# Kernel tuning notes

Measured on AMD Instinct MI355X. Metric: run time of the kernel, lower is better.

Reference implementation:

```python
import jax, jax.numpy as jnp
import numpy as np

B, NF, E, T, M = 4096, 50, 64, 2, 3
LN_EPS = 1e-5
NEG_INF = -1e9


def _xavier_uniform(k, shape, fan_in, fan_out):
    a = float(np.sqrt(6.0 / (fan_in + fan_out)))
    return jax.random.uniform(k, shape, jnp.float32, -a, a)


def setup_inputs() -> dict:
    key = jax.random.key(0)
    ks = jax.random.split(key, 6)
    feat = jax.random.normal(ks[0], (B, NF, E), jnp.float32)
    masker = _xavier_uniform(ks[1], (T, M, NF, NF), NF, NF)
    transform_w = _xavier_uniform(ks[2], (1, T, 1, 2 * E, E), 2 * E, E)
    transform_b = _xavier_uniform(ks[3], (T, 1, NF, E), NF, E)
    ln_w = jnp.ones((NF,), jnp.float32)
    ln_b = jnp.zeros((NF,), jnp.float32)
    gating_w = jax.random.normal(ks[4], (NF * E, 1), jnp.float32) / np.sqrt(NF * E)
    gating_b = jnp.zeros((1,), jnp.float32)
    return {
        "feat": feat,
        "masker": masker,
        "transform_w": transform_w,
        "transform_b": transform_b,
        "ln_w": ln_w,
        "ln_b": ln_b,
        "gating_w": gating_w,
        "gating_b": gating_b,
    }


def reference(feat, masker, transform_w, transform_b, ln_w, ln_b, gating_w, gating_b):
    b, nf, e = feat.shape
    t = masker.shape[0]
    # hop adjacency: product of masks, relu'd  (T, F, F)
    adj = jax.nn.relu(jnp.prod(masker, axis=1))
    mask = (adj != 0).astype(feat.dtype)
    # LayerNorm(num_fields) applied on transposed adj == normalize over axis -2,
    # with gamma/beta broadcasting along the normalized (row) axis.
    mean = adj.mean(axis=-2, keepdims=True)
    var = adj.var(axis=-2, keepdims=True)
    adj_ln = (adj - mean) / jnp.sqrt(var + LN_EPS) * ln_w[:, None] + ln_b[:, None]
    logits = adj_ln + (1.0 - mask) * NEG_INF + jnp.eye(nf, dtype=feat.dtype)
    # softmax over dim=1 of (T, F, F) == axis -2 (rows), then re-mask
    attn = jax.nn.softmax(logits, axis=-2) * mask
    # nei[b,t,g,e] = sum_f feat[b,f,e] * attn[t,f,g]
    nei = jnp.einsum('bfe,tfg->btge', feat, attn)  # (B, T, F, E)
    x = jnp.broadcast_to(feat[:, None], (b, t, nf, e))
    cat = jnp.concatenate([x, nei], axis=-1)  # (B, T, F, 2E)
    w0 = transform_w[0, :, 0]                 # (T, 2E, E)  (idx=0 slice)
    h = jnp.einsum('btfk,tke->btfe', cat, w0) + transform_b[:, 0]  # (B,T,F,E)
    flat = h.reshape(b, t, nf * e)
    gate = jax.nn.softmax(flat @ gating_w + gating_b, axis=1)  # (B, T, 1)
    out = jnp.sum(flat * gate, axis=1).reshape(b, nf, e)
    return out
```

## Files before the change

kernel.cpp:

```cpp
#include <hip/hip_runtime.h>
#include <hip/hip_bf16.h>

#define NFEAT 50
#define EDIM 64
#define LN_EPS 1e-5f
#define NEG_INF_C (-1000000000.0f)
#define NB 4

typedef __bf16 bf16_t;
typedef __bf16 bf16x8 __attribute__((ext_vector_type(8)));
typedef __bf16 bf16x4 __attribute__((ext_vector_type(4)));
typedef float f32x4 __attribute__((ext_vector_type(4)));

#define MFMA __builtin_amdgcn_mfma_f32_16x16x32_bf16


__global__ __launch_bounds__(256) void prep_kernel(
    const float* __restrict__ masker, const float* __restrict__ ln_w,
    const float* __restrict__ ln_b, const float* __restrict__ tw,
    const float* __restrict__ tb, const float* __restrict__ gw,
    bf16_t* __restrict__ ws_attnT, bf16_t* __restrict__ ws_WT,
    float* __restrict__ ws_tbT, float* __restrict__ ws_gwT,
    float* __restrict__ ws_cst)
{
  __shared__ float red[2][4];
  const int tid = threadIdx.x;
  const int lane = tid & 63;
  const int gidx = blockIdx.x * 256 + tid;

#pragma unroll
  for (int j = 0; j < 4; ++j) {
    int o = gidx * 4 + j;
    int kl = o & 63;
    int e = (o >> 6) & 63;
    int ti = o >> 12;
    int k = ((kl >> 3) ^ (e & 7)) * 8 + (kl & 7);
    ws_WT[o] = (bf16_t)tw[(ti * 64 + k) * 64 + e];
  }

#pragma unroll
  for (int j = 0; j < 2; ++j) {
    int o = gidx * 2 + j;
    int f = o & 63;
    int e = (o >> 6) & 63;
    int t = o >> 12;
    ws_tbT[o] = (f < NFEAT) ? tb[(t * NFEAT + f) * EDIM + e] : 0.f;
  }

  {
    int o = gidx;
    int f = o & 63;
    int e = o >> 6;
    ws_gwT[o] = (f < NFEAT) ? gw[f * EDIM + e] : 0.f;
  }

  if (blockIdx.x == 0) {
    float s0 = 0.f, s1 = 0.f;
    for (int i = tid; i < NFEAT * EDIM; i += 256) {
      float g = gw[i];
      s0 += tb[i] * g;
      s1 += tb[NFEAT * EDIM + i] * g;
    }
    for (int off = 32; off > 0; off >>= 1) {
      s0 += __shfl_xor(s0, off);
      s1 += __shfl_xor(s1, off);
    }
    if (lane == 0) { red[0][tid >> 6] = s0; red[1][tid >> 6] = s1; }
    __syncthreads();
    if (tid == 0) {
      ws_cst[0] = red[0][0] + red[0][1] + red[0][2] + red[0][3];
      ws_cst[1] = red[1][0] + red[1][1] + red[1][2] + red[1][3];
    }
  }

  const int wg = blockIdx.x * 4 + (tid >> 6);
  const int f = lane;
  const bool fv = (f < NFEAT);
  for (int i = 0; i < 2; ++i) {
    int col = wg * 2 + i;
    int t = col >> 6, g = col & 63;
    float val = 0.f;
    if (fv && g < NFEAT) {
      float a0 = masker[((t * 3 + 0) * NFEAT + f) * NFEAT + g];
      float a1 = masker[((t * 3 + 1) * NFEAT + f) * NFEAT + g];
      float a2 = masker[((t * 3 + 2) * NFEAT + f) * NFEAT + g];
      float prod = a0 * a1 * a2;
      val = prod > 0.f ? prod : 0.f;
    }
    float s = val;
    for (int off = 32; off > 0; off >>= 1) s += __shfl_xor(s, off);
    float mean = s / (float)NFEAT;
    float d = fv ? (val - mean) : 0.f;
    float v2 = d * d;
    for (int off = 32; off > 0; off >>= 1) v2 += __shfl_xor(v2, off);
    float var = v2 / (float)NFEAT;
    float lw = fv ? ln_w[f] : 0.f;
    float lb = fv ? ln_b[f] : 0.f;
    float aln = d * rsqrtf(var + LN_EPS) * lw + lb;
    float logit = aln + ((val != 0.f) ? 0.f : NEG_INF_C) + ((f == g) ? 1.f : 0.f);
    if (!fv) logit = -3.0e38f;
    float mx = logit;
    for (int off = 32; off > 0; off >>= 1) mx = fmaxf(mx, __shfl_xor(mx, off));
    float ex = fv ? expf(logit - mx) : 0.f;
    float se = ex;
    for (int off = 32; off > 0; off >>= 1) se += __shfl_xor(se, off);
    float attn = (fv && g < NFEAT && val != 0.f) ? (ex / se) : 0.f;
    ws_attnT[(t * 64 + g) * 64 + f] = (bf16_t)attn;
  }
}

__global__ __launch_bounds__(256) void main_kernel(
    const float* __restrict__ feat, const float* __restrict__ gb,
    const bf16_t* __restrict__ ws_attnT, const bf16_t* __restrict__ ws_WT,
    const float* __restrict__ ws_tbT, const float* __restrict__ ws_gwT,
    const float* __restrict__ ws_cst,
    float* __restrict__ out)
{
  __shared__ bf16_t sWT[4 * 64 * 64];
  __shared__ bf16_t sPT[2][64 * 64];
  __shared__ float sLog[2][4];

  const int tid = threadIdx.x;
  const int w = tid >> 6;
  const int lane = tid & 63;
  const int l16 = lane & 15;
  const int lquad = lane >> 4;
  const int m0 = w * 16;

#pragma unroll
  for (int it = 0; it < 8; ++it) {
    const int idx = it * 256 + tid;
    *(bf16x8*)&sWT[idx * 8] = *(const bf16x8*)(ws_WT + idx * 8);
  }

  bf16x8 aat[2][2];
#pragma unroll
  for (int t = 0; t < 2; ++t)
#pragma unroll
    for (int kc = 0; kc < 2; ++kc)
      aat[t][kc] = *(const bf16x8*)(ws_attnT + (t * 64 + m0 + l16) * 64 + kc * 32 + lquad * 8);

  const float cst0 = ws_cst[0], cst1 = ws_cst[1], gbv = gb[0];
  const int fA = m0 + l16;
  const bool fAv = (fA < NFEAT);
  const int b0 = blockIdx.x * NB;
  const int foff = fA * 64 + lquad * 8;
  const int exl = l16 & 7;
  const int wcl = (m0 >> 3) + (lquad >> 1);
  const int whf = (lquad & 1) * 4;

  f32x4 raw[4];
  if (fAv) {
    const float* fb = feat + b0 * (NFEAT * EDIM) + foff;
    raw[0] = *(const f32x4*)(fb);
    raw[1] = *(const f32x4*)(fb + 4);
    raw[2] = *(const f32x4*)(fb + 32);
    raw[3] = *(const f32x4*)(fb + 36);
  }

  __syncthreads();

#pragma unroll 1
  for (int ib = 0; ib < NB; ++ib) {
    const int b = b0 + ib;

    bf16x8 a[2];
#pragma unroll
    for (int kc = 0; kc < 2; ++kc)
#pragma unroll
      for (int j = 0; j < 8; ++j) a[kc][j] = (bf16_t)0.f;
    if (fAv) {
#pragma unroll
      for (int j = 0; j < 4; ++j) {
        a[0][j] = (bf16_t)raw[0][j]; a[0][j + 4] = (bf16_t)raw[1][j];
        a[1][j] = (bf16_t)raw[2][j]; a[1][j + 4] = (bf16_t)raw[3][j];
      }
    }

    f32x4 accH[2][4], accP[2][4];
#pragma unroll
    for (int t = 0; t < 2; ++t)
#pragma unroll
      for (int n = 0; n < 4; ++n) {
        accH[t][n] = (f32x4){0.f, 0.f, 0.f, 0.f};
        accP[t][n] = (f32x4){0.f, 0.f, 0.f, 0.f};
      }

#pragma unroll
    for (int kc = 0; kc < 2; ++kc) {
      const int co = ((kc * 4 + lquad) ^ exl) * 8;
#pragma unroll
      for (int n = 0; n < 4; ++n) {
        const int ro = (n * 16 + l16) * 64 + co;
        const bf16x8 b10 = *(const bf16x8*)(&sWT[0 * 4096 + ro]);
        const bf16x8 b20 = *(const bf16x8*)(&sWT[1 * 4096 + ro]);
        const bf16x8 b11 = *(const bf16x8*)(&sWT[2 * 4096 + ro]);
        const bf16x8 b21 = *(const bf16x8*)(&sWT[3 * 4096 + ro]);
        accH[0][n] = MFMA(a[kc], b10, accH[0][n], 0, 0, 0);
        accP[0][n] = MFMA(a[kc], b20, accP[0][n], 0, 0, 0);
        accH[1][n] = MFMA(a[kc], b11, accH[1][n], 0, 0, 0);
        accP[1][n] = MFMA(a[kc], b21, accP[1][n], 0, 0, 0);
      }
    }

#pragma unroll
    for (int t = 0; t < 2; ++t)
#pragma unroll
      for (int n = 0; n < 4; ++n) {
        bf16x4 pv;
        pv[0] = (bf16_t)accP[t][n][0]; pv[1] = (bf16_t)accP[t][n][1];
        pv[2] = (bf16_t)accP[t][n][2]; pv[3] = (bf16_t)accP[t][n][3];
        *(bf16x4*)&sPT[t][(n * 16 + l16) * 64 + ((wcl ^ exl) << 3) + whf] = pv;
      }
    __syncthreads();

    if (ib + 1 < NB && fAv) {
      const float* fb = feat + (b + 1) * (NFEAT * EDIM) + foff;
      raw[0] = *(const f32x4*)(fb);
      raw[1] = *(const f32x4*)(fb + 4);
      raw[2] = *(const f32x4*)(fb + 32);
      raw[3] = *(const f32x4*)(fb + 36);
    }

#pragma unroll
    for (int kc = 0; kc < 2; ++kc) {
      const int so0 = ((kc * 4 + lquad) ^ exl) << 3;
#pragma unroll
      for (int n = 0; n < 4; ++n) {
        const int so = (n * 16 + l16) * 64 + so0;
        const bf16x8 bp0 = *(const bf16x8*)(&sPT[0][so]);
        const bf16x8 bp1 = *(const bf16x8*)(&sPT[1][so]);
        accH[0][n] = MFMA(aat[0][kc], bp0, accH[0][n], 0, 0, 0);
        accH[1][n] = MFMA(aat[1][kc], bp1, accH[1][n], 0, 0, 0);
      }
    }

    float p0 = 0.f, p1 = 0.f;
#pragma unroll
    for (int n = 0; n < 4; ++n) {
      const f32x4 gwv = *(const f32x4*)(ws_gwT + (n * 16 + l16) * 64 + m0 + lquad * 4);
#pragma unroll
      for (int r = 0; r < 4; ++r) {
        p0 += accH[0][n][r] * gwv[r];
        p1 += accH[1][n][r] * gwv[r];
      }
    }
#pragma unroll
    for (int off = 32; off > 0; off >>= 1) {
      p0 += __shfl_xor(p0, off);
      p1 += __shfl_xor(p1, off);
    }
    if (lane == 0) { sLog[0][w] = p0; sLog[1][w] = p1; }
    __syncthreads();

    const float g0 = sLog[0][0] + sLog[0][1] + sLog[0][2] + sLog[0][3] + cst0 + gbv;
    const float g1 = sLog[1][0] + sLog[1][1] + sLog[1][2] + sLog[1][3] + cst1 + gbv;
    const float mx = fmaxf(g0, g1);
    const float e0 = expf(g0 - mx), e1 = expf(g1 - mx);
    const float inv = 1.f / (e0 + e1);
    const float ga0 = e0 * inv, ga1 = e1 * inv;

    float* outb = out + b * (NFEAT * EDIM);
#pragma unroll
    for (int n = 0; n < 4; ++n) {
      const int ro = (n * 16 + l16) * 64 + m0 + lquad * 4;
      const f32x4 tbv0 = *(const f32x4*)(ws_tbT + ro);
      const f32x4 tbv1 = *(const f32x4*)(ws_tbT + 64 * 64 + ro);
      const int e = n * 16 + l16;
#pragma unroll
      for (int r = 0; r < 4; ++r) {
        const int f = m0 + lquad * 4 + r;
        if (f < NFEAT)
          outb[f * 64 + e] = ga0 * (accH[0][n][r] + tbv0[r])
                           + ga1 * (accH[1][n][r] + tbv1[r]);
      }
    }
  }
}

extern "C" void kernel_launch(void* const* d_in, const int* in_sizes, int n_in,
                              void* d_out, int out_size, void* d_ws, size_t ws_size,
                              hipStream_t stream) {
  const float* feat   = (const float*)d_in[0];
  const float* masker = (const float*)d_in[1];
  const float* tw     = (const float*)d_in[2];
  const float* tb     = (const float*)d_in[3];
  const float* lnw    = (const float*)d_in[4];
  const float* lnb    = (const float*)d_in[5];
  const float* gw     = (const float*)d_in[6];
  const float* gb     = (const float*)d_in[7];
  float* out = (float*)d_out;

  bf16_t* ws_attnT = (bf16_t*)d_ws;
  bf16_t* ws_WT    = ws_attnT + 2 * 64 * 64;
  float*  ws_tbT   = (float*)(ws_WT + 4 * 64 * 64);
  float*  ws_gwT   = ws_tbT + 2 * 64 * 64;
  float*  ws_cst   = ws_gwT + 64 * 64;

  prep_kernel<<<16, 256, 0, stream>>>(masker, lnw, lnb, tw, tb, gw,
                                      ws_attnT, ws_WT, ws_tbT, ws_gwT, ws_cst);
  main_kernel<<<4096 / NB, 256, 0, stream>>>(feat, gb, ws_attnT, ws_WT,
                                             ws_tbT, ws_gwT, ws_cst, out);
}
```

Before: 140.7 us.

## Precompute folded gating weights so gate logits come directly from raw features

```diff
diff --git a/kernel.cpp b/kernel.cpp
--- a/kernel.cpp
+++ b/kernel.cpp
@@ -14,13 +14,20 @@
 
 #define MFMA __builtin_amdgcn_mfma_f32_16x16x32_bf16
 
+__device__ __forceinline__ void lds_barrier() {
+  asm volatile("s_waitcnt lgkmcnt(0)" ::: "memory");
+  __builtin_amdgcn_sched_barrier(0);
+  __builtin_amdgcn_s_barrier();
+  __builtin_amdgcn_sched_barrier(0);
+}
+
 
 __global__ __launch_bounds__(256) void prep_kernel(
     const float* __restrict__ masker, const float* __restrict__ ln_w,
     const float* __restrict__ ln_b, const float* __restrict__ tw,
     const float* __restrict__ tb, const float* __restrict__ gw,
     bf16_t* __restrict__ ws_attnT, bf16_t* __restrict__ ws_WT,
-    float* __restrict__ ws_tbT, float* __restrict__ ws_gwT,
+    float* __restrict__ ws_tbT, float* __restrict__ ws_attnF,
     float* __restrict__ ws_cst)
 {
   __shared__ float red[2][4];
@@ -45,13 +52,6 @@
     int e = (o >> 6) & 63;
     int t = o >> 12;
     ws_tbT[o] = (f < NFEAT) ? tb[(t * NFEAT + f) * EDIM + e] : 0.f;
-  }
-
-  {
-    int o = gidx;
-    int f = o & 63;
-    int e = o >> 6;
-    ws_gwT[o] = (f < NFEAT) ? gw[f * EDIM + e] : 0.f;
   }
 
   if (blockIdx.x == 0) {
@@ -106,13 +106,107 @@
     for (int off = 32; off > 0; off >>= 1) se += __shfl_xor(se, off);
     float attn = (fv && g < NFEAT && val != 0.f) ? (ex / se) : 0.f;
     ws_attnT[(t * 64 + g) * 64 + f] = (bf16_t)attn;
-  }
+    ws_attnF[(t * 64 + f) * 64 + g] = attn;
+  }
+}
+
+__global__ __launch_bounds__(256) void prep2_kernel(
+    const float* __restrict__ tw, const float* __restrict__ gw,
+    const float* __restrict__ ws_attnF, float* __restrict__ ws_G)
+{
+  __shared__ bf16_t sRT[64 * 72];
+  const int t = blockIdx.x;
+  const int tid = threadIdx.x;
+  const int w = tid >> 6;
+  const int lane = tid & 63;
+  const int l16 = lane & 15;
+  const int lquad = lane >> 4;
+  const int fr = w * 16 + l16;
+  const bool frv = (fr < NFEAT);
+
+  bf16x8 ag[2];
+#pragma unroll
+  for (int kc = 0; kc < 2; ++kc) {
+#pragma unroll
+    for (int j = 0; j < 8; ++j) ag[kc][j] = (bf16_t)0.f;
+    if (frv) {
+      const float* p = gw + fr * 64 + kc * 32 + lquad * 8;
+      const f32x4 r0 = *(const f32x4*)(p);
+      const f32x4 r1 = *(const f32x4*)(p + 4);
+#pragma unroll
+      for (int j = 0; j < 4; ++j) { ag[kc][j] = (bf16_t)r0[j]; ag[kc][j+4] = (bf16_t)r1[j]; }
+    }
+  }
+
+  f32x4 accR[4];
+#pragma unroll
+  for (int n = 0; n < 4; ++n) accR[n] = (f32x4){0.f,0.f,0.f,0.f};
+#pragma unroll
+  for (int kc = 0; kc < 2; ++kc)
+#pragma unroll
+    for (int n = 0; n < 4; ++n) {
+      const float* p = tw + ((2*t+1)*64 + n*16 + l16) * 64 + kc*32 + lquad*8;
+      const f32x4 r0 = *(const f32x4*)(p);
+      const f32x4 r1 = *(const f32x4*)(p + 4);
+      bf16x8 bw;
+#pragma unroll
+      for (int j = 0; j < 4; ++j) { bw[j] = (bf16_t)r0[j]; bw[j+4] = (bf16_t)r1[j]; }
+      accR[n] = MFMA(ag[kc], bw, accR[n], 0, 0, 0);
+    }
+#pragma unroll
+  for (int n = 0; n < 4; ++n) {
+    bf16x4 pv;
+    pv[0]=(bf16_t)accR[n][0]; pv[1]=(bf16_t)accR[n][1];
+    pv[2]=(bf16_t)accR[n][2]; pv[3]=(bf16_t)accR[n][3];
+    *(bf16x4*)&sRT[(n*16 + l16) * 72 + w*16 + lquad*4] = pv;
+  }
+
+  f32x4 acc[4];
+#pragma unroll
+  for (int n = 0; n < 4; ++n) acc[n] = (f32x4){0.f,0.f,0.f,0.f};
+#pragma unroll
+  for (int kc = 0; kc < 2; ++kc)
+#pragma unroll
+    for (int n = 0; n < 4; ++n) {
+      const float* p = tw + ((2*t)*64 + n*16 + l16) * 64 + kc*32 + lquad*8;
+      const f32x4 r0 = *(const f32x4*)(p);
+      const f32x4 r1 = *(const f32x4*)(p + 4);
+      bf16x8 bw;
+#pragma unroll
+      for (int j = 0; j < 4; ++j) { bw[j] = (bf16_t)r0[j]; bw[j+4] = (bf16_t)r1[j]; }
+      acc[n] = MFMA(ag[kc], bw, acc[n], 0, 0, 0);
+    }
+
+  __syncthreads();
+
+  bf16x8 aa[2];
+#pragma unroll
+  for (int kc = 0; kc < 2; ++kc) {
+    const float* p = ws_attnF + (t*64 + fr) * 64 + kc*32 + lquad*8;
+    const f32x4 r0 = *(const f32x4*)(p);
+    const f32x4 r1 = *(const f32x4*)(p + 4);
+#pragma unroll
+    for (int j = 0; j < 4; ++j) { aa[kc][j] = (bf16_t)r0[j]; aa[kc][j+4] = (bf16_t)r1[j]; }
+  }
+#pragma unroll
+  for (int kc = 0; kc < 2; ++kc)
+#pragma unroll
+    for (int n = 0; n < 4; ++n) {
+      const bf16x8 bp = *(const bf16x8*)(&sRT[(n*16 + l16) * 72 + kc*32 + lquad*8]);
+      acc[n] = MFMA(aa[kc], bp, acc[n], 0, 0, 0);
+    }
+
+#pragma unroll
+  for (int n = 0; n < 4; ++n)
+#pragma unroll
+    for (int r = 0; r < 4; ++r)
+      ws_G[t*4096 + (w*16 + lquad*4 + r) * 64 + n*16 + l16] = acc[n][r];
 }
 
 __global__ __launch_bounds__(256) void main_kernel(
     const float* __restrict__ feat, const float* __restrict__ gb,
     const bf16_t* __restrict__ ws_attnT, const bf16_t* __restrict__ ws_WT,
-    const float* __restrict__ ws_tbT, const float* __restrict__ ws_gwT,
+    const float* __restrict__ ws_tbT, const float* __restrict__ ws_G,
     const float* __restrict__ ws_cst,
     float* __restrict__ out)
 {
@@ -149,7 +243,19 @@
   const int wcl = (m0 >> 3) + (lquad >> 1);
   const int whf = (lquad & 1) * 4;
 
+  f32x4 gfr[2][4];
+#pragma unroll
+  for (int t = 0; t < 2; ++t) {
+    const float* gp = ws_G + t * 4096 + foff;
+    gfr[t][0] = *(const f32x4*)(gp);
+    gfr[t][1] = *(const f32x4*)(gp + 4);
+    gfr[t][2] = *(const f32x4*)(gp + 32);
+    gfr[t][3] = *(const f32x4*)(gp + 36);
+  }
+
   f32x4 raw[4];
+#pragma unroll
+  for (int i = 0; i < 4; ++i) raw[i] = (f32x4){0.f, 0.f, 0.f, 0.f};
   if (fAv) {
     const float* fb = feat + b0 * (NFEAT * EDIM) + foff;
     raw[0] = *(const f32x4*)(fb);
@@ -158,7 +264,7 @@
     raw[3] = *(const f32x4*)(fb + 36);
   }
 
-  __syncthreads();
+  lds_barrier();
 
 #pragma unroll 1
   for (int ib = 0; ib < NB; ++ib) {
@@ -175,6 +281,23 @@
         a[0][j] = (bf16_t)raw[0][j]; a[0][j + 4] = (bf16_t)raw[1][j];
         a[1][j] = (bf16_t)raw[2][j]; a[1][j + 4] = (bf16_t)raw[3][j];
       }
+    }
+
+    float p0 = 0.f, p1 = 0.f;
+#pragma unroll
+    for (int q = 0; q < 4; ++q)
+#pragma unroll
+      for (int j = 0; j < 4; ++j) {
+        p0 += raw[q][j] * gfr[0][q][j];
+        p1 += raw[q][j] * gfr[1][q][j];
+      }
+
+    if (ib + 1 < NB && fAv) {
+      const float* fb = feat + (b + 1) * (NFEAT * EDIM) + foff;
+      raw[0] = *(const f32x4*)(fb);
+      raw[1] = *(const f32x4*)(fb + 4);
+      raw[2] = *(const f32x4*)(fb + 32);
+      raw[3] = *(const f32x4*)(fb + 36);
     }
 
     f32x4 accH[2][4], accP[2][4];
@@ -204,6 +327,13 @@
     }
 
 #pragma unroll
+    for (int off = 32; off > 0; off >>= 1) {
+      p0 += __shfl_xor(p0, off);
+      p1 += __shfl_xor(p1, off);
+    }
+    if (lane == 0) { sLog[0][w] = p0; sLog[1][w] = p1; }
+
+#pragma unroll
     for (int t = 0; t < 2; ++t)
 #pragma unroll
       for (int n = 0; n < 4; ++n) {
@@ -212,15 +342,15 @@
         pv[2] = (bf16_t)accP[t][n][2]; pv[3] = (bf16_t)accP[t][n][3];
         *(bf16x4*)&sPT[t][(n * 16 + l16) * 64 + ((wcl ^ exl) << 3) + whf] = pv;
       }
-    __syncthreads();
-
-    if (ib + 1 < NB && fAv) {
-      const float* fb = feat + (b + 1) * (NFEAT * EDIM) + foff;
-      raw[0] = *(const f32x4*)(fb);
-      raw[1] = *(const f32x4*)(fb + 4);
-      raw[2] = *(const f32x4*)(fb + 32);
-      raw[3] = *(const f32x4*)(fb + 36);
-    }
+
+    lds_barrier();
+
+    const float g0 = sLog[0][0] + sLog[0][1] + sLog[0][2] + sLog[0][3] + cst0 + gbv;
+    const float g1 = sLog[1][0] + sLog[1][1] + sLog[1][2] + sLog[1][3] + cst1 + gbv;
+    const float mx = fmaxf(g0, g1);
+    const float e0 = expf(g0 - mx), e1 = expf(g1 - mx);
+    const float inv = 1.f / (e0 + e1);
+    const float ga0 = e0 * inv, ga1 = e1 * inv;
 
 #pragma unroll
     for (int kc = 0; kc < 2; ++kc) {
@@ -235,30 +365,7 @@
       }
     }
 
-    float p0 = 0.f, p1 = 0.f;
-#pragma unroll
-    for (int n = 0; n < 4; ++n) {
-      const f32x4 gwv = *(const f32x4*)(ws_gwT + (n * 16 + l16) * 64 + m0 + lquad * 4);
-#pragma unroll
-      for (int r = 0; r < 4; ++r) {
-        p0 += accH[0][n][r] * gwv[r];
-        p1 += accH[1][n][r] * gwv[r];
-      }
-    }
-#pragma unroll
-    for (int off = 32; off > 0; off >>= 1) {
-      p0 += __shfl_xor(p0, off);
-      p1 += __shfl_xor(p1, off);
-    }
-    if (lane == 0) { sLog[0][w] = p0; sLog[1][w] = p1; }
-    __syncthreads();
-
-    const float g0 = sLog[0][0] + sLog[0][1] + sLog[0][2] + sLog[0][3] + cst0 + gbv;
-    const float g1 = sLog[1][0] + sLog[1][1] + sLog[1][2] + sLog[1][3] + cst1 + gbv;
-    const float mx = fmaxf(g0, g1);
-    const float e0 = expf(g0 - mx), e1 = expf(g1 - mx);
-    const float inv = 1.f / (e0 + e1);
-    const float ga0 = e0 * inv, ga1 = e1 * inv;
+    lds_barrier();
 
     float* outb = out + b * (NFEAT * EDIM);
 #pragma unroll
@@ -292,13 +399,15 @@
   float* out = (float*)d_out;
 
   bf16_t* ws_attnT = (bf16_t*)d_ws;
-  bf16_t* ws_WT    = ws_attnT + 2 * 64 * 64;
-  float*  ws_tbT   = (float*)(ws_WT + 4 * 64 * 64);
-  float*  ws_gwT   = ws_tbT + 2 * 64 * 64;
-  float*  ws_cst   = ws_gwT + 64 * 64;
+  bf16_t* ws_WT    = ws_attnT + 8192;
+  float*  ws_tbT   = (float*)(ws_WT + 16384);
+  float*  ws_attnF = ws_tbT + 8192;
+  float*  ws_G     = ws_attnF + 8192;
+  float*  ws_cst   = ws_G + 8192;
 
   prep_kernel<<<16, 256, 0, stream>>>(masker, lnw, lnb, tw, tb, gw,
-                                      ws_attnT, ws_WT, ws_tbT, ws_gwT, ws_cst);
+                                      ws_attnT, ws_WT, ws_tbT, ws_attnF, ws_cst);
+  prep2_kernel<<<2, 256, 0, stream>>>(tw, gw, ws_attnF, ws_G);
   main_kernel<<<4096 / NB, 256, 0, stream>>>(feat, gb, ws_attnT, ws_WT,
-                                             ws_tbT, ws_gwT, ws_cst, out);
+                                             ws_tbT, ws_G, ws_cst, out);
 }
```

New measurement: 164.9 us. 17.2% more time.
